# Optimization experiments

Measured on AMD Instinct MI355X. Metric: run time of the kernel, lower is better.

The kernel has to match this reference:

```python
import jax, jax.numpy as jnp
import numpy as np

B, D, E, C = 16384, 768, 124, 6  # batch, emb_dim, n_experts, n_classes


def _mlp(h, w1, b1, w2, b2):
    # timm Mlp: fc1 -> GELU(exact) -> fc2, hidden = in_features
    return jax.nn.gelu(h @ w1 + b1, approximate=False) @ w2 + b2


def setup_inputs() -> dict:
    key = jax.random.key(0)
    ks = jax.random.split(key, 14)
    s = 0.02
    inp = {
        "x": jax.random.normal(ks[0], (B, D), dtype=jnp.float32),
        # per-sample expert counts in [1, E]
        "n_experts": jax.random.randint(ks[1], (B,), 1, E + 1, dtype=jnp.int64 if jax.config.jax_enable_x64 else jnp.int32),
        # classifier Mlp: D -> D -> E*C
        "cls_w1": jax.random.normal(ks[2], (D, D), dtype=jnp.float32) * s,
        "cls_b1": jnp.zeros((D,), jnp.float32),
        "cls_w2": jax.random.normal(ks[3], (D, E * C), dtype=jnp.float32) * s,
        "cls_b2": jnp.zeros((E * C,), jnp.float32),
        # which_expert Mlp: D -> D -> E
        "we_w1": jax.random.normal(ks[4], (D, D), dtype=jnp.float32) * s,
        "we_b1": jnp.zeros((D,), jnp.float32),
        "we_w2": jax.random.normal(ks[5], (D, E), dtype=jnp.float32) * s,
        "we_b2": jnp.zeros((E,), jnp.float32),
        # expert_weights Mlp: D -> D -> E
        "ew_w1": jax.random.normal(ks[6], (D, D), dtype=jnp.float32) * s,
        "ew_b1": jnp.zeros((D,), jnp.float32),
        "ew_w2": jax.random.normal(ks[7], (D, E), dtype=jnp.float32) * s,
        "ew_b2": jnp.zeros((E,), jnp.float32),
    }
    return inp


def reference(x, n_experts, cls_w1, cls_b1, cls_w2, cls_b2,
              we_w1, we_b1, we_w2, we_b2, ew_w1, ew_b1, ew_w2, ew_b2):
    emb = x  # backbone = identity
    expert_logits = _mlp(emb, cls_w1, cls_b1, cls_w2, cls_b2).reshape(B, E, C)
    expert_weight_logits = _mlp(emb, ew_w1, ew_b1, ew_w2, ew_b2)  # [B, E]
    which_expert = _mlp(emb, we_w1, we_b1, we_w2, we_b2)          # [B, E]

    n = jnp.minimum(n_experts, E)                                  # clamp to n_experts
    # kth_largest: sort descending, pick (n-1)-th per row -> threshold
    sorted_desc = -jnp.sort(-which_expert, axis=1)
    threshold = sorted_desc[jnp.arange(B), n - 1][:, None]         # [B, 1]
    mask = which_expert < threshold

    expert_weight_logits = jnp.where(mask, -jnp.inf, expert_weight_logits)
    expert_proba = jax.nn.softmax(expert_logits, axis=2)           # over classes
    expert_weights = jax.nn.softmax(expert_weight_logits, axis=1)  # over experts

    combined = (expert_proba * expert_weights[:, :, None]).sum(axis=1)
    return combined / expert_weights.sum(axis=1)[:, None]          # [B, C]
```

## Files before the change

### kernel.cpp

```cpp
#include <hip/hip_runtime.h>
#include <stdint.h>

typedef unsigned short u16;
typedef short short8 __attribute__((ext_vector_type(8)));
typedef float f32x4 __attribute__((ext_vector_type(4)));

#define NB 16384

#define OFF_XHI      0ull
#define OFF_XLO      25165824ull
#define OFF_LCLS     0ull
#define OFF_BT1      50331648ull
#define OFF_LEWB     50331648ull
#define OFF_BTWE_HI  52690944ull
#define OFF_BTWE_LO  53870592ull
#define OFF_BT2CLS   55050240ull
#define OFF_BT2EW    56229888ull
#define OFF_BT2WE_HI 56426496ull
#define OFF_BT2WE_LO 56623104ull
#define OFF_B1CE     56819712ull
#define OFF_B1WE     56825856ull
#define OFF_B2CLS    56828928ull
#define OFF_B2EW     56832000ull
#define OFF_B2WE     56832512ull
#define OFF_HCLSEW   56833024ull
#define OFF_PWE      107164672ull
#define WS_NEED      157496320ull
#define PWE_STRIDE   2097152ull

__device__ __forceinline__ u16 f2bf(float f) {
  uint32_t u = __float_as_uint(f);
  u += 0x7fffu + ((u >> 16) & 1u);
  return (u16)(u >> 16);
}
__device__ __forceinline__ float bf2f(u16 h) {
  return __uint_as_float(((uint32_t)h) << 16);
}
__device__ __forceinline__ uint32_t pk2(float a, float b) {
  return (uint32_t)f2bf(a) | ((uint32_t)f2bf(b) << 16);
}
__device__ __forceinline__ void g2l16(const u16* g, u16* l) {
  __builtin_amdgcn_global_load_lds(
      (__attribute__((address_space(1))) void*)(u16*)g,
      (__attribute__((address_space(3))) void*)l, 16, 0, 0);
}

__device__ __forceinline__ float gelu_exact(float v) {
  const float x = fabsf(v) * 0.70710678118654752f;
  const float t = __fdividef(1.0f, __builtin_fmaf(0.3275911f, x, 1.0f));
  float p = __builtin_fmaf(1.061405429f, t, -1.453152027f);
  p = __builtin_fmaf(p, t, 1.421413741f);
  p = __builtin_fmaf(p, t, -0.284496736f);
  p = __builtin_fmaf(p, t, 0.254829592f);
  p = p * t;
  const float e = __expf(-x * x);
  float erfx = __builtin_fmaf(-p, e, 1.0f);
  erfx = (v < 0.f) ? -erfx : erfx;
  return 0.5f * v * (1.0f + erfx);
}

__global__ void prep_all(
    const float* __restrict__ x, u16* __restrict__ xhi, u16* __restrict__ xlo,
    const float* __restrict__ cls_w1, const float* __restrict__ ew_w1,
    const float* __restrict__ we_w1,  const float* __restrict__ cls_w2,
    const float* __restrict__ ew_w2,  const float* __restrict__ we_w2,
    u16* BT1, u16* BTwe_hi, u16* BTwe_lo,
    u16* BT2cls, u16* BT2ew, u16* BT2we_hi, u16* BT2we_lo,
    const float* __restrict__ cls_b1, const float* __restrict__ ew_b1,
    const float* __restrict__ we_b1,  const float* __restrict__ cls_b2,
    const float* __restrict__ ew_b2,  const float* __restrict__ we_b2,
    float* b1ce, float* b1we, float* b2cls, float* b2ew, float* b2we) {
  __shared__ float t[64][65];
  const int bid = blockIdx.x;
  if (bid < 12288) {
    int i = bid * 256 + threadIdx.x;
    float4 v = ((const float4*)x)[i];
    ushort4 h, l;
    h.x = f2bf(v.x); l.x = f2bf(v.x - bf2f(h.x));
    h.y = f2bf(v.y); l.y = f2bf(v.y - bf2f(h.y));
    h.z = f2bf(v.z); l.z = f2bf(v.z - bf2f(h.z));
    h.w = f2bf(v.w); l.w = f2bf(v.w - bf2f(h.w));
    ((ushort4*)xhi)[i] = h;
    ((ushort4*)xlo)[i] = l;
    return;
  }
  if (bid < 13152) {
    const int idx = bid - 12288;
    const int bx = idx % 12, by = (idx / 12) % 12, bz = idx / 144;
    const float* src; int N; u16* dhi; u16* dlo = nullptr;
    switch (bz) {
      case 0: src = cls_w1; N = 768; dhi = BT1; break;
      case 1: src = ew_w1;  N = 768; dhi = BT1 + 768 * 768; break;
      case 2: src = we_w1;  N = 768; dhi = BTwe_hi; dlo = BTwe_lo; break;
      case 3: src = cls_w2; N = 744; dhi = BT2cls; break;
      case 4: src = ew_w2;  N = 124; dhi = BT2ew; break;
      default: src = we_w2; N = 124; dhi = BT2we_hi; dlo = BT2we_lo; break;
    }
    const int Npad = (N + 127) & ~127;
    const int n0 = by * 64;
    if (n0 >= Npad) return;
    const int k0 = bx * 64;
    const int tx = threadIdx.x & 63, tg = threadIdx.x >> 6;
#pragma unroll
    for (int r = 0; r < 16; ++r) {
      int k = tg * 16 + r;
      int n = n0 + tx;
      t[k][tx] = (n < N) ? src[(size_t)(k0 + k) * N + n] : 0.f;
    }
    __syncthreads();
#pragma unroll
    for (int r = 0; r < 16; ++r) {
      int n = n0 + tg * 16 + r;
      if (n < Npad) {
        float v = t[tx][tg * 16 + r];
        u16 h = f2bf(v);
        dhi[(size_t)n * 768 + k0 + tx] = h;
        if (dlo) dlo[(size_t)n * 768 + k0 + tx] = f2bf(v - bf2f(h));
      }
    }
    return;
  }
  int id = (bid - 13152) * 256 + threadIdx.x;
  if (id < 1536) { b1ce[id] = (id < 768) ? cls_b1[id] : ew_b1[id - 768]; return; }
  id -= 1536;
  if (id < 768) { b1we[id] = we_b1[id]; return; }
  id -= 768;
  if (id < 768) { b2cls[id] = (id < 744) ? cls_b2[id] : 0.f; return; }
  id -= 768;
  if (id < 128) { b2ew[id] = (id < 124) ? ew_b2[id] : 0.f; return; }
  id -= 128;
  if (id < 128) { b2we[id] = (id < 124) ? we_b2[id] : 0.f; return; }
}

__device__ __forceinline__ void gemm_core(
    const u16* A0, int lda,
    const u16* B0,
    int K, int bm, int tid, u16* sA, u16* sB, f32x4 acc[4][4]) {
  const int lane = tid & 63;
  const int wv = tid >> 6;
  const int wr = wv >> 1, wc = wv & 1;
  const int sr = lane >> 3;
  const int sc = (((lane & 7) ^ sr) << 3);
  const u16* gA = A0 + (size_t)(bm + wv * 32 + sr) * lda + sc;
  const u16* gB = B0 + (size_t)(wv * 32 + sr) * K + sc;
  u16* lA = sA + (wv * 32) * 64;
  u16* lB = sB + (wv * 32) * 64;
  for (int kt = 0; kt < K; kt += 64) {
#pragma unroll
    for (int s = 0; s < 4; ++s) {
      g2l16(gA + (size_t)(s * 8) * lda + kt, lA + s * 8 * 64);
      g2l16(gB + (size_t)(s * 8) * K + kt, lB + s * 8 * 64);
    }
    __syncthreads();
#pragma unroll
    for (int ks = 0; ks < 2; ++ks) {
      const int co = ((ks * 4 + (lane >> 4)) ^ (lane & 7)) * 8;
      short8 av[4], bv[4];
#pragma unroll
      for (int i = 0; i < 4; i++)
        av[i] = *(const short8*)(sA + (wr * 64 + i * 16 + (lane & 15)) * 64 + co);
#pragma unroll
      for (int j = 0; j < 4; j++)
        bv[j] = *(const short8*)(sB + (wc * 64 + j * 16 + (lane & 15)) * 64 + co);
#pragma unroll
      for (int i = 0; i < 4; i++)
#pragma unroll
        for (int j = 0; j < 4; j++)
          acc[i][j] = __builtin_amdgcn_mfma_f32_16x16x32_bf16(bv[j], av[i], acc[i][j], 0, 0, 0);
    }
    __syncthreads();
  }
}

__device__ __forceinline__ void gemm_split_core(
    const u16* __restrict__ Ahi, const u16* __restrict__ Alo, int lda,
    const u16* __restrict__ Bhi, const u16* __restrict__ Blo, int ldb,
    int K, int bm, int tid, u16* sA, u16* sB, f32x4 acc[4][4]) {
  const int lane = tid & 63;
  const int wv = tid >> 6;
  const int wr = wv >> 1, wc = wv & 1;
  const int sr = lane >> 3;
  const int gl = (lane & 7) ^ sr;
  const int koff = (gl & 3) << 3;
  const u16* Asel = (gl < 4) ? Ahi : Alo;
  const u16* Bsel = (gl < 4) ? Bhi : Blo;
  const u16* gA = Asel + (size_t)(bm + wv * 32 + sr) * lda + koff;
  const u16* gB = Bsel + (size_t)(wv * 32 + sr) * ldb + koff;
  u16* lA = sA + (wv * 32) * 64;
  u16* lB = sB + (wv * 32) * 64;

  for (int kt = 0; kt < K; kt += 32) {
#pragma unroll
    for (int s = 0; s < 4; ++s) {
      g2l16(gA + (size_t)(s * 8) * lda + kt, lA + s * 8 * 64);
      g2l16(gB + (size_t)(s * 8) * ldb + kt, lB + s * 8 * 64);
    }
    __syncthreads();
    const int coh = (((lane >> 4) ^ (lane & 7)) << 3);
    short8 ah[4], al[4], bh[4], bl[4];
#pragma unroll
    for (int i = 0; i < 4; i++) {
      const u16* p = sA + (wr * 64 + i * 16 + (lane & 15)) * 64;
      ah[i] = *(const short8*)(p + coh);
      al[i] = *(const short8*)(p + (coh ^ 32));
    }
#pragma unroll
    for (int j = 0; j < 4; j++) {
      const u16* p = sB + (wc * 64 + j * 16 + (lane & 15)) * 64;
      bh[j] = *(const short8*)(p + coh);
      bl[j] = *(const short8*)(p + (coh ^ 32));
    }
#pragma unroll
    for (int i = 0; i < 4; i++)
#pragma unroll
      for (int j = 0; j < 4; j++) {
        acc[i][j] = __builtin_amdgcn_mfma_f32_16x16x32_bf16(bh[j], ah[i], acc[i][j], 0, 0, 0);
        acc[i][j] = __builtin_amdgcn_mfma_f32_16x16x32_bf16(bh[j], al[i], acc[i][j], 0, 0, 0);
        acc[i][j] = __builtin_amdgcn_mfma_f32_16x16x32_bf16(bl[j], ah[i], acc[i][j], 0, 0, 0);
      }
    __syncthreads();
  }
}

__device__ __forceinline__ void decode_bid(int bid, int NC, int& bm, int& bn) {
  const int xcd = bid & 7, slot = bid >> 3;
  const int per = NC << 3;
  const int sub = slot / per, rem = slot - sub * per;
  const int colu = rem >> 3, rowIn = rem & 7;
  bm = ((xcd << 4) + (sub << 3) + rowIn) << 7;
  bn = colu << 7;
}

__global__ __launch_bounds__(256, 3) void gemm1_fused(
    const u16* __restrict__ Ahi, const u16* __restrict__ Alo,
    const u16* __restrict__ Bwe_hi, const u16* __restrict__ Bwe_lo,
    const u16* __restrict__ BT1,
    const float* __restrict__ b1we, const float* __restrict__ b1ce,
    const u16* __restrict__ BT2we_hi, const u16* __restrict__ BT2we_lo,
    const float* __restrict__ b2we,
    float* __restrict__ pwe,
    u16* __restrict__ out_ce) {
  __shared__ u16 smem[2 * 128 * 64];
  u16* sA = smem;
  u16* sB = smem + 128 * 64;
  const int tid = threadIdx.x;
  const int lane = tid & 63;
  const int wv = tid >> 6;
  const int wr = wv >> 1, wc = wv & 1;
  const int K = 768;

  f32x4 acc[4][4];
#pragma unroll
  for (int i = 0; i < 4; i++)
#pragma unroll
    for (int j = 0; j < 4; j++) acc[i][j] = f32x4{0.f, 0.f, 0.f, 0.f};

  if (blockIdx.x < 768) {
    int bm, bn;
    decode_bid(blockIdx.x, 6, bm, bn);
    gemm_split_core(Ahi, Alo, K, Bwe_hi + (size_t)bn * K, Bwe_lo + (size_t)bn * K, K,
                    K, bm, tid, sA, sB, acc);

    const int lg4 = (lane >> 4) << 2;
    const int sr = lane >> 3;
    const int gl = (lane & 7) ^ sr;
    const int koff = (gl & 3) << 3;
    const u16* Bsel2 = (gl < 4) ? BT2we_hi : BT2we_lo;
    const u16* gB2 = Bsel2 + (size_t)(wv * 32 + sr) * 768 + bn + koff;
    u16* lB = sB + (wv * 32) * 64;
    const int coh = (((lane >> 4) ^ (lane & 7)) << 3);

    f32x4 acc2[4][4];
#pragma unroll
    for (int i = 0; i < 4; i++)
#pragma unroll
      for (int j = 0; j < 4; j++) acc2[i][j] = f32x4{0.f, 0.f, 0.f, 0.f};

#pragma unroll
    for (int c = 0; c < 4; ++c) {
#pragma unroll
      for (int s = 0; s < 4; ++s)
        g2l16(gB2 + (size_t)(s * 8) * 768 + (c << 5), lB + s * 8 * 64);
      if (wc == (c >> 1)) {
#pragma unroll
        for (int i = 0; i < 4; i++) {
          const int row = wr * 64 + i * 16 + (lane & 15);
          const int rs = row & 7;
          u16* lrow = sA + row * 64;
#pragma unroll
          for (int jj = 0; jj < 2; jj++) {
            const int j = ((c & 1) << 1) + jj;
            const int col = bn + wc * 64 + j * 16 + lg4;
            const float4 bs = *(const float4*)(b1we + col);
            float g0 = gelu_exact(acc[i][j][0] + bs.x);
            float g1 = gelu_exact(acc[i][j][1] + bs.y);
            float g2 = gelu_exact(acc[i][j][2] + bs.z);
            float g3 = gelu_exact(acc[i][j][3] + bs.w);
            u16 h0 = f2bf(g0), h1 = f2bf(g1), h2 = f2bf(g2), h3 = f2bf(g3);
            uint2 hv, lv;
            hv.x = (uint32_t)h0 | ((uint32_t)h1 << 16);
            hv.y = (uint32_t)h2 | ((uint32_t)h3 << 16);
            lv.x = pk2(g0 - bf2f(h0), g1 - bf2f(h1));
            lv.y = pk2(g2 - bf2f(h2), g3 - bf2f(h3));
            const int kk = ((j & 1) << 4) + lg4;
            const int gr = kk >> 3;
            const int off = kk & 7;
            *(uint2*)(lrow + ((gr ^ rs) << 3) + off) = hv;
            *(uint2*)(lrow + (((gr ^ rs) ^ 4) << 3) + off) = lv;
          }
        }
      }
      __syncthreads();
      short8 ah[4], al[4], bh[4], bl[4];
#pragma unroll
      for (int i = 0; i < 4; i++) {
        const u16* p = sA + (wr * 64 + i * 16 + (lane & 15)) * 64;
        ah[i] = *(const short8*)(p + coh);
        al[i] = *(const short8*)(p + (coh ^ 32));
      }
#pragma unroll
      for (int j = 0; j < 4; j++) {
        const u16* p = sB + (wc * 64 + j * 16 + (lane & 15)) * 64;
        bh[j] = *(const short8*)(p + coh);
        bl[j] = *(const short8*)(p + (coh ^ 32));
      }
#pragma unroll
      for (int i = 0; i < 4; i++)
#pragma unroll
        for (int j = 0; j < 4; j++) {
          acc2[i][j] = __builtin_amdgcn_mfma_f32_16x16x32_bf16(bh[j], ah[i], acc2[i][j], 0, 0, 0);
          acc2[i][j] = __builtin_amdgcn_mfma_f32_16x16x32_bf16(bh[j], al[i], acc2[i][j], 0, 0, 0);
          acc2[i][j] = __builtin_amdgcn_mfma_f32_16x16x32_bf16(bl[j], ah[i], acc2[i][j], 0, 0, 0);
        }
      __syncthreads();
    }
    const int t = bn >> 7;
    float* pw = pwe + (size_t)t * PWE_STRIDE;
#pragma unroll
    for (int i = 0; i < 4; i++) {
      const int row = bm + wr * 64 + i * 16 + (lane & 15);
#pragma unroll
      for (int j = 0; j < 4; j++) {
        const int e0 = wc * 64 + j * 16 + lg4;
        float4 v = make_float4(acc2[i][j][0], acc2[i][j][1], acc2[i][j][2], acc2[i][j][3]);
        if (t == 0) {
          const float4 bs = *(const float4*)(b2we + e0);
          v.x += bs.x; v.y += bs.y; v.z += bs.z; v.w += bs.w;
        }
        *(float4*)(pw + (size_t)row * 128 + e0) = v;
      }
    }
  } else {
    int bm, bn;
    decode_bid(blockIdx.x - 768, 12, bm, bn);
    gemm_core(Ahi, 768, BT1 + (size_t)bn * K, K, bm, tid, sA, sB, acc);
    const int lg4 = (lane >> 4) << 2;
#pragma unroll
    for (int i = 0; i < 4; i++) {
      const int row = bm + wr * 64 + i * 16 + (lane & 15);
      u16* ro = out_ce + (size_t)row * 1536;
#pragma unroll
      for (int j = 0; j < 4; j++) {
        const int colb = bn + wc * 64 + j * 16 + lg4;
        const float4 bs = *(const float4*)(b1ce + colb);
        uint2 hv;
        hv.x = pk2(gelu_exact(acc[i][j][0] + bs.x), gelu_exact(acc[i][j][1] + bs.y));
        hv.y = pk2(gelu_exact(acc[i][j][2] + bs.z), gelu_exact(acc[i][j][3] + bs.w));
        *(uint2*)(ro + colb) = hv;
      }
    }
  }
}

__global__ __launch_bounds__(256, 4) void gemm2_fused(
    const u16* __restrict__ h_cls,
    const u16* __restrict__ BT2cls, const u16* __restrict__ BT2ew,
    const float* __restrict__ b2cls, const float* __restrict__ b2ew,
    u16* __restrict__ Lcls, u16* __restrict__ LewB) {
  __shared__ u16 sA[128 * 64];
  __shared__ u16 sB[128 * 64];
  const int tid = threadIdx.x;
  const int lane = tid & 63;
  const int wr = (tid >> 6) >> 1, wc = (tid >> 6) & 1;
  const int lg4 = (lane >> 4) << 2;

  f32x4 acc[4][4];
#pragma unroll
  for (int i = 0; i < 4; i++)
#pragma unroll
    for (int j = 0; j < 4; j++) acc[i][j] = f32x4{0.f, 0.f, 0.f, 0.f};

  const int bid = blockIdx.x;
  if (bid < 768) {
    int bm, bn;
    decode_bid(bid, 6, bm, bn);
    gemm_core(h_cls, 1536, BT2cls + (size_t)bn * 768, 768, bm, tid, sA, sB, acc);
#pragma unroll
    for (int i = 0; i < 4; i++) {
      const int row = bm + wr * 64 + i * 16 + (lane & 15);
      u16* ro = Lcls + (size_t)row * 768;
#pragma unroll
      for (int j = 0; j < 4; j++) {
        const int colb = bn + wc * 64 + j * 16 + lg4;
        const float4 bs = *(const float4*)(b2cls + colb);
        uint2 hv;
        hv.x = pk2(acc[i][j][0] + bs.x, acc[i][j][1] + bs.y);
        hv.y = pk2(acc[i][j][2] + bs.z, acc[i][j][3] + bs.w);
        *(uint2*)(ro + colb) = hv;
      }
    }
  } else {
    const int r = bid - 768;
    const int bm = (((r & 7) << 4) + (r >> 3)) << 7;
    gemm_core(h_cls + 768, 1536, BT2ew, 768, bm, tid, sA, sB, acc);
#pragma unroll
    for (int i = 0; i < 4; i++) {
      const int row = bm + wr * 64 + i * 16 + (lane & 15);
      u16* ro = LewB + (size_t)row * 128;
#pragma unroll
      for (int j = 0; j < 4; j++) {
        const int colb = wc * 64 + j * 16 + lg4;
        const float4 bs = *(const float4*)(b2ew + colb);
        uint2 hv;
        hv.x = pk2(acc[i][j][0] + bs.x, acc[i][j][1] + bs.y);
        hv.y = pk2(acc[i][j][2] + bs.z, acc[i][j][3] + bs.w);
        *(uint2*)(ro + colb) = hv;
      }
    }
  }
}

__global__ __launch_bounds__(256) void finalize(
    const u16* __restrict__ Lcls,
    const float* __restrict__ pwe,
    const u16* __restrict__ LewB,
    const int* __restrict__ nexp, float* __restrict__ out) {
  const int bid = blockIdx.x;
  const int g = ((bid & 7) << 9) + (bid >> 3);
  const int b = (g << 2) + (int)(threadIdx.x >> 6);
  const int lane = threadIdx.x & 63;
  const float NEG = -3.0e38f;
  const size_t base = (size_t)b * 128;
  float w0 = NEG, w1 = NEG;
  if (lane < 124) {
    const float* q = pwe + base + lane;
    w0 = q[0] + q[PWE_STRIDE] + q[2 * PWE_STRIDE] + q[3 * PWE_STRIDE]
       + q[4 * PWE_STRIDE] + q[5 * PWE_STRIDE];
  }
  if (lane < 60) {
    const float* q = pwe + base + 64 + lane;
    w1 = q[0] + q[PWE_STRIDE] + q[2 * PWE_STRIDE] + q[3 * PWE_STRIDE]
       + q[4 * PWE_STRIDE] + q[5 * PWE_STRIDE];
  }
  int r0 = 0, r1 = 0;
#pragma unroll
  for (int j = 0; j < 64; ++j) {
    float v = __shfl(w0, j, 64);
    r0 += (v > w0); r1 += (v > w1);
  }
#pragma unroll
  for (int j = 0; j < 64; ++j) {
    float v = __shfl(w1, j, 64);
    r0 += (v > w0); r1 += (v > w1);
  }
  int n = nexp[b];
  n = n < 1 ? 1 : (n > 124 ? 124 : n);
  const bool k0 = (lane < 124) && (r0 < n);
  const bool k1 = (lane < 60) && (r1 < n);
  float l0 = k0 ? bf2f(LewB[base + lane]) : NEG;
  float l1 = k1 ? bf2f(LewB[base + 64 + lane]) : NEG;
  float mx = fmaxf(l0, l1);
#pragma unroll
  for (int o = 32; o > 0; o >>= 1) mx = fmaxf(mx, __shfl_xor(mx, o, 64));
  float e0 = k0 ? __expf(l0 - mx) : 0.f;
  float e1 = k1 ? __expf(l1 - mx) : 0.f;
  float S = e0 + e1;
#pragma unroll
  for (int o = 32; o > 0; o >>= 1) S += __shfl_xor(S, o, 64);
  float a0 = 0, a1 = 0, a2 = 0, a3 = 0, a4 = 0, a5 = 0;
#pragma unroll
  for (int h = 0; h < 2; ++h) {
    int e = lane + h * 64;
    float we = h ? e1 : e0;
    if (we > 0.f) {
      const u16* lp = Lcls + (size_t)b * 768 + e * 6;
      float c0 = bf2f(lp[0]), c1 = bf2f(lp[1]), c2 = bf2f(lp[2]);
      float c3 = bf2f(lp[3]), c4 = bf2f(lp[4]), c5 = bf2f(lp[5]);
      float m = fmaxf(fmaxf(fmaxf(c0, c1), fmaxf(c2, c3)), fmaxf(c4, c5));
      float q0 = __expf(c0 - m), q1 = __expf(c1 - m), q2 = __expf(c2 - m);
      float q3 = __expf(c3 - m), q4 = __expf(c4 - m), q5 = __expf(c5 - m);
      float inv = we / (q0 + q1 + q2 + q3 + q4 + q5);
      a0 += q0 * inv; a1 += q1 * inv; a2 += q2 * inv;
      a3 += q3 * inv; a4 += q4 * inv; a5 += q5 * inv;
    }
  }
#pragma unroll
  for (int o = 32; o > 0; o >>= 1) {
    a0 += __shfl_xor(a0, o, 64); a1 += __shfl_xor(a1, o, 64);
    a2 += __shfl_xor(a2, o, 64); a3 += __shfl_xor(a3, o, 64);
    a4 += __shfl_xor(a4, o, 64); a5 += __shfl_xor(a5, o, 64);
  }
  if (lane < 6) {
    float v = (lane == 0) ? a0 : (lane == 1) ? a1 : (lane == 2) ? a2
              : (lane == 3) ? a3 : (lane == 4) ? a4 : a5;
    out[(size_t)b * 6 + lane] = v / S;
  }
}

__global__ void fill_sentinel(float* out, int n, float v) {
  int i = blockIdx.x * 256 + threadIdx.x;
  if (i < n) out[i] = v;
}

extern "C" void kernel_launch(void* const* d_in, const int* in_sizes, int n_in,
                              void* d_out, int out_size, void* d_ws, size_t ws_size,
                              hipStream_t stream) {
  const float* x = (const float*)d_in[0];
  const int* nexp = (const int*)d_in[1];
  const float* cls_w1 = (const float*)d_in[2];
  const float* cls_b1 = (const float*)d_in[3];
  const float* cls_w2 = (const float*)d_in[4];
  const float* cls_b2 = (const float*)d_in[5];
  const float* we_w1 = (const float*)d_in[6];
  const float* we_b1 = (const float*)d_in[7];
  const float* we_w2 = (const float*)d_in[8];
  const float* we_b2 = (const float*)d_in[9];
  const float* ew_w1 = (const float*)d_in[10];
  const float* ew_b1 = (const float*)d_in[11];
  const float* ew_w2 = (const float*)d_in[12];
  const float* ew_b2 = (const float*)d_in[13];
  float* out = (float*)d_out;
  char* ws = (char*)d_ws;

  if (ws_size < WS_NEED) {
    fill_sentinel<<<(out_size + 255) / 256, 256, 0, stream>>>(out, out_size, 12345.0f);
    return;
  }

  u16* xhi = (u16*)(ws + OFF_XHI);
  u16* xlo = (u16*)(ws + OFF_XLO);
  u16* Lcls = (u16*)(ws + OFF_LCLS);
  u16* LewB = (u16*)(ws + OFF_LEWB);
  u16* BT1 = (u16*)(ws + OFF_BT1);
  u16* BTwe_hi = (u16*)(ws + OFF_BTWE_HI);
  u16* BTwe_lo = (u16*)(ws + OFF_BTWE_LO);
  u16* BT2cls = (u16*)(ws + OFF_BT2CLS);
  u16* BT2ew = (u16*)(ws + OFF_BT2EW);
  u16* BT2we_hi = (u16*)(ws + OFF_BT2WE_HI);
  u16* BT2we_lo = (u16*)(ws + OFF_BT2WE_LO);
  float* b1ce = (float*)(ws + OFF_B1CE);
  float* b1we = (float*)(ws + OFF_B1WE);
  float* b2cls = (float*)(ws + OFF_B2CLS);
  float* b2ew = (float*)(ws + OFF_B2EW);
  float* b2we = (float*)(ws + OFF_B2WE);
  u16* h_clsew = (u16*)(ws + OFF_HCLSEW);
  float* pwe = (float*)(ws + OFF_PWE);

  prep_all<<<13165, 256, 0, stream>>>(x, xhi, xlo,
                                      cls_w1, ew_w1, we_w1, cls_w2, ew_w2, we_w2,
                                      BT1, BTwe_hi, BTwe_lo, BT2cls, BT2ew, BT2we_hi, BT2we_lo,
                                      cls_b1, ew_b1, we_b1, cls_b2, ew_b2, we_b2,
                                      b1ce, b1we, b2cls, b2ew, b2we);
  gemm1_fused<<<2304, 256, 0, stream>>>(xhi, xlo, BTwe_hi, BTwe_lo, BT1,
                                        b1we, b1ce, BT2we_hi, BT2we_lo, b2we,
                                        pwe, h_clsew);
  gemm2_fused<<<896, 256, 0, stream>>>(h_clsew, BT2cls, BT2ew,
                                       b2cls, b2ew, Lcls, LewB);
  finalize<<<4096, 256, 0, stream>>>(Lcls, pwe, LewB, nexp, out);
}
```

Measured before the change: 346.0 us.

## Accumulate which_expert second GEMM across hidden tiles inside one block

The which_expert branch used 768 blocks, each writing a partial second-layer product for one 128-wide hidden tile to six separate buffers. It now uses 128 blocks that loop over all six hidden tiles and keep the second-layer accumulator in registers. This removes the partial-sum buffers, their global writes, and the six-way reduction in finalize. In exchange, far fewer and much longer blocks handle this branch, which risks poor load balance and a long serial tail relative to the classifier blocks.

New measurement: 505.6 us. +46.1%, slower.

```diff
diff --git a/kernel.cpp b/kernel.cpp
--- a/kernel.cpp
+++ b/kernel.cpp
@@ -26,7 +26,6 @@
 #define OFF_HCLSEW   56833024ull
 #define OFF_PWE      107164672ull
 #define WS_NEED      157496320ull
-#define PWE_STRIDE   2097152ull
 
 __device__ __forceinline__ u16 f2bf(float f) {
   uint32_t u = __float_as_uint(f);
@@ -255,18 +254,15 @@
 #pragma unroll
     for (int j = 0; j < 4; j++) acc[i][j] = f32x4{0.f, 0.f, 0.f, 0.f};
 
-  if (blockIdx.x < 768) {
-    int bm, bn;
-    decode_bid(blockIdx.x, 6, bm, bn);
-    gemm_split_core(Ahi, Alo, K, Bwe_hi + (size_t)bn * K, Bwe_lo + (size_t)bn * K, K,
-                    K, bm, tid, sA, sB, acc);
+  if (blockIdx.x < 128) {
+    const int r = blockIdx.x;
+    const int bm = (((r & 7) << 4) + (r >> 3)) << 7;
 
     const int lg4 = (lane >> 4) << 2;
     const int sr = lane >> 3;
     const int gl = (lane & 7) ^ sr;
     const int koff = (gl & 3) << 3;
     const u16* Bsel2 = (gl < 4) ? BT2we_hi : BT2we_lo;
-    const u16* gB2 = Bsel2 + (size_t)(wv * 32 + sr) * 768 + bn + koff;
     u16* lB = sB + (wv * 32) * 64;
     const int coh = (((lane >> 4) ^ (lane & 7)) << 3);
 
@@ -276,83 +272,91 @@
 #pragma unroll
       for (int j = 0; j < 4; j++) acc2[i][j] = f32x4{0.f, 0.f, 0.f, 0.f};
 
-#pragma unroll
-    for (int c = 0; c < 4; ++c) {
-#pragma unroll
-      for (int s = 0; s < 4; ++s)
-        g2l16(gB2 + (size_t)(s * 8) * 768 + (c << 5), lB + s * 8 * 64);
-      if (wc == (c >> 1)) {
-#pragma unroll
-        for (int i = 0; i < 4; i++) {
-          const int row = wr * 64 + i * 16 + (lane & 15);
-          const int rs = row & 7;
-          u16* lrow = sA + row * 64;
-#pragma unroll
-          for (int jj = 0; jj < 2; jj++) {
-            const int j = ((c & 1) << 1) + jj;
-            const int col = bn + wc * 64 + j * 16 + lg4;
-            const float4 bs = *(const float4*)(b1we + col);
-            float g0 = gelu_exact(acc[i][j][0] + bs.x);
-            float g1 = gelu_exact(acc[i][j][1] + bs.y);
-            float g2 = gelu_exact(acc[i][j][2] + bs.z);
-            float g3 = gelu_exact(acc[i][j][3] + bs.w);
-            u16 h0 = f2bf(g0), h1 = f2bf(g1), h2 = f2bf(g2), h3 = f2bf(g3);
-            uint2 hv, lv;
-            hv.x = (uint32_t)h0 | ((uint32_t)h1 << 16);
-            hv.y = (uint32_t)h2 | ((uint32_t)h3 << 16);
-            lv.x = pk2(g0 - bf2f(h0), g1 - bf2f(h1));
-            lv.y = pk2(g2 - bf2f(h2), g3 - bf2f(h3));
-            const int kk = ((j & 1) << 4) + lg4;
-            const int gr = kk >> 3;
-            const int off = kk & 7;
-            *(uint2*)(lrow + ((gr ^ rs) << 3) + off) = hv;
-            *(uint2*)(lrow + (((gr ^ rs) ^ 4) << 3) + off) = lv;
+#pragma unroll 1
+    for (int t = 0; t < 6; ++t) {
+      const int bn = t << 7;
+#pragma unroll
+      for (int i = 0; i < 4; i++)
+#pragma unroll
+        for (int j = 0; j < 4; j++) acc[i][j] = f32x4{0.f, 0.f, 0.f, 0.f};
+      gemm_split_core(Ahi, Alo, K, Bwe_hi + (size_t)bn * K, Bwe_lo + (size_t)bn * K, K,
+                      K, bm, tid, sA, sB, acc);
+
+      const u16* gB2 = Bsel2 + (size_t)(wv * 32 + sr) * 768 + bn + koff;
+#pragma unroll
+      for (int c = 0; c < 4; ++c) {
+#pragma unroll
+        for (int s = 0; s < 4; ++s)
+          g2l16(gB2 + (size_t)(s * 8) * 768 + (c << 5), lB + s * 8 * 64);
+        if (wc == (c >> 1)) {
+#pragma unroll
+          for (int i = 0; i < 4; i++) {
+            const int row = wr * 64 + i * 16 + (lane & 15);
+            const int rs = row & 7;
+            u16* lrow = sA + row * 64;
+#pragma unroll
+            for (int jj = 0; jj < 2; jj++) {
+              const int j = ((c & 1) << 1) + jj;
+              const int col = bn + wc * 64 + j * 16 + lg4;
+              const float4 bs = *(const float4*)(b1we + col);
+              float g0 = gelu_exact(acc[i][j][0] + bs.x);
+              float g1 = gelu_exact(acc[i][j][1] + bs.y);
+              float g2 = gelu_exact(acc[i][j][2] + bs.z);
+              float g3 = gelu_exact(acc[i][j][3] + bs.w);
+              u16 h0 = f2bf(g0), h1 = f2bf(g1), h2 = f2bf(g2), h3 = f2bf(g3);
+              uint2 hv, lv;
+              hv.x = (uint32_t)h0 | ((uint32_t)h1 << 16);
+              hv.y = (uint32_t)h2 | ((uint32_t)h3 << 16);
+              lv.x = pk2(g0 - bf2f(h0), g1 - bf2f(h1));
+              lv.y = pk2(g2 - bf2f(h2), g3 - bf2f(h3));
+              const int kk = ((j & 1) << 4) + lg4;
+              const int gr = kk >> 3;
+              const int off = kk & 7;
+              *(uint2*)(lrow + ((gr ^ rs) << 3) + off) = hv;
+              *(uint2*)(lrow + (((gr ^ rs) ^ 4) << 3) + off) = lv;
+            }
           }
         }
-      }
-      __syncthreads();
-      short8 ah[4], al[4], bh[4], bl[4];
-#pragma unroll
-      for (int i = 0; i < 4; i++) {
-        const u16* p = sA + (wr * 64 + i * 16 + (lane & 15)) * 64;
-        ah[i] = *(const short8*)(p + coh);
-        al[i] = *(const short8*)(p + (coh ^ 32));
-      }
-#pragma unroll
-      for (int j = 0; j < 4; j++) {
-        const u16* p = sB + (wc * 64 + j * 16 + (lane & 15)) * 64;
-        bh[j] = *(const short8*)(p + coh);
-        bl[j] = *(const short8*)(p + (coh ^ 32));
-      }
-#pragma unroll
-      for (int i = 0; i < 4; i++)
+        __syncthreads();
+        short8 ah[4], al[4], bh[4], bl[4];
+#pragma unroll
+        for (int i = 0; i < 4; i++) {
+          const u16* p = sA + (wr * 64 + i * 16 + (lane & 15)) * 64;
+          ah[i] = *(const short8*)(p + coh);
+          al[i] = *(const short8*)(p + (coh ^ 32));
+        }
 #pragma unroll
         for (int j = 0; j < 4; j++) {
-          acc2[i][j] = __builtin_amdgcn_mfma_f32_16x16x32_bf16(bh[j], ah[i], acc2[i][j], 0, 0, 0);
-          acc2[i][j] = __builtin_amdgcn_mfma_f32_16x16x32_bf16(bh[j], al[i], acc2[i][j], 0, 0, 0);
-          acc2[i][j] = __builtin_amdgcn_mfma_f32_16x16x32_bf16(bl[j], ah[i], acc2[i][j], 0, 0, 0);
+          const u16* p = sB + (wc * 64 + j * 16 + (lane & 15)) * 64;
+          bh[j] = *(const short8*)(p + coh);
+          bl[j] = *(const short8*)(p + (coh ^ 32));
         }
-      __syncthreads();
-    }
-    const int t = bn >> 7;
-    float* pw = pwe + (size_t)t * PWE_STRIDE;
+#pragma unroll
+        for (int i = 0; i < 4; i++)
+#pragma unroll
+          for (int j = 0; j < 4; j++) {
+            acc2[i][j] = __builtin_amdgcn_mfma_f32_16x16x32_bf16(bh[j], ah[i], acc2[i][j], 0, 0, 0);
+            acc2[i][j] = __builtin_amdgcn_mfma_f32_16x16x32_bf16(bh[j], al[i], acc2[i][j], 0, 0, 0);
+            acc2[i][j] = __builtin_amdgcn_mfma_f32_16x16x32_bf16(bl[j], ah[i], acc2[i][j], 0, 0, 0);
+          }
+        __syncthreads();
+      }
+    }
 #pragma unroll
     for (int i = 0; i < 4; i++) {
       const int row = bm + wr * 64 + i * 16 + (lane & 15);
 #pragma unroll
       for (int j = 0; j < 4; j++) {
         const int e0 = wc * 64 + j * 16 + lg4;
-        float4 v = make_float4(acc2[i][j][0], acc2[i][j][1], acc2[i][j][2], acc2[i][j][3]);
-        if (t == 0) {
-          const float4 bs = *(const float4*)(b2we + e0);
-          v.x += bs.x; v.y += bs.y; v.z += bs.z; v.w += bs.w;
-        }
-        *(float4*)(pw + (size_t)row * 128 + e0) = v;
+        const float4 bs = *(const float4*)(b2we + e0);
+        float4 v = make_float4(acc2[i][j][0] + bs.x, acc2[i][j][1] + bs.y,
+                               acc2[i][j][2] + bs.z, acc2[i][j][3] + bs.w);
+        *(float4*)(pwe + (size_t)row * 128 + e0) = v;
       }
     }
   } else {
     int bm, bn;
-    decode_bid(blockIdx.x - 768, 12, bm, bn);
+    decode_bid(blockIdx.x - 128, 12, bm, bn);
     gemm_core(Ahi, 768, BT1 + (size_t)bn * K, K, bm, tid, sA, sB, acc);
     const int lg4 = (lane >> 4) << 2;
 #pragma unroll
@@ -441,17 +445,8 @@
   const int lane = threadIdx.x & 63;
   const float NEG = -3.0e38f;
   const size_t base = (size_t)b * 128;
-  float w0 = NEG, w1 = NEG;
-  if (lane < 124) {
-    const float* q = pwe + base + lane;
-    w0 = q[0] + q[PWE_STRIDE] + q[2 * PWE_STRIDE] + q[3 * PWE_STRIDE]
-       + q[4 * PWE_STRIDE] + q[5 * PWE_STRIDE];
-  }
-  if (lane < 60) {
-    const float* q = pwe + base + 64 + lane;
-    w1 = q[0] + q[PWE_STRIDE] + q[2 * PWE_STRIDE] + q[3 * PWE_STRIDE]
-       + q[4 * PWE_STRIDE] + q[5 * PWE_STRIDE];
-  }
+  const float w0 = (lane < 124) ? pwe[base + lane] : NEG;
+  const float w1 = (lane < 60) ? pwe[base + 64 + lane] : NEG;
   int r0 = 0, r1 = 0;
 #pragma unroll
   for (int j = 0; j < 64; ++j) {
@@ -561,7 +556,7 @@
                                       BT1, BTwe_hi, BTwe_lo, BT2cls, BT2ew, BT2we_hi, BT2we_lo,
                                       cls_b1, ew_b1, we_b1, cls_b2, ew_b2, we_b2,
                                       b1ce, b1we, b2cls, b2ew, b2we);
-  gemm1_fused<<<2304, 256, 0, stream>>>(xhi, xlo, BTwe_hi, BTwe_lo, BT1,
+  gemm1_fused<<<1664, 256, 0, stream>>>(xhi, xlo, BTwe_hi, BTwe_lo, BT1,
                                         b1we, b1ce, BT2we_hi, BT2we_lo, b2we,
                                         pwe, h_clsew);
   gemm2_fused<<<896, 256, 0, stream>>>(h_clsew, BT2cls, BT2ew,
```
